# Kernel tuning notes

Measured on AMD Instinct MI355X. Metric: run time of the kernel, lower is better.

The kernel has to match this reference:

```python
import jax, jax.numpy as jnp
import numpy as np
import math

B, S, D, H = 2, 2048, 1024, 16
DH = D // H

def setup_inputs() -> dict:
    key = jax.random.key(0)
    ks = jax.random.split(key, 12)
    s = 1.0 / math.sqrt(D)
    return {
        "q": jax.random.normal(ks[0], (B, S, D), jnp.float32),
        "k": jax.random.normal(ks[1], (B, S, D), jnp.float32),
        "v": jax.random.normal(ks[2], (B, S, D), jnp.float32),
        "mask": jnp.tril(jnp.ones((S, S), dtype=bool)),  # causal mask
        "Wq": jax.random.normal(ks[3], (D, D), jnp.float32) * s,
        "bq": jnp.zeros((D,), jnp.float32),
        "Wk": jax.random.normal(ks[4], (D, D), jnp.float32) * s,
        "bk": jnp.zeros((D,), jnp.float32),
        "Wv": jax.random.normal(ks[5], (D, D), jnp.float32) * s,
        "bv": jnp.zeros((D,), jnp.float32),
        "Wo": jax.random.normal(ks[6], (D, D), jnp.float32) * s,
        "bo": jnp.zeros((D,), jnp.float32),
    }

def _split_heads(x):
    b, s, _ = x.shape
    return x.reshape(b, s, H, DH).transpose(0, 2, 1, 3)  # [B,H,S,DH]

def reference(q, k, v, mask, Wq, bq, Wk, bk, Wv, bv, Wo, bo):
    qh = _split_heads(q @ Wq.T + bq)
    kh = _split_heads(k @ Wk.T + bk)
    vh = _split_heads(v @ Wv.T + bv)
    scale = 1.0 / math.sqrt(DH)
    scores = jnp.einsum('bhqd,bhkd->bhqk', qh, kh) * scale  # [B,H,S,S]
    scores = jnp.where(mask[None, None, :, :], scores, -jnp.inf)
    attn = jax.nn.softmax(scores, axis=-1)
    out = jnp.einsum('bhqk,bhkd->bhqd', attn, vh)  # [B,H,S,DH]
    out = out.transpose(0, 2, 1, 3).reshape(B, S, D)  # combine heads
    return out @ Wo.T + bo
```

## Files before the change

### kernel.cpp

```cpp
#include <hip/hip_runtime.h>

typedef unsigned int u32;
typedef unsigned short u16;
typedef __attribute__((ext_vector_type(8))) short bf16x8;
typedef __attribute__((ext_vector_type(8))) u16 u16x8;
typedef __attribute__((ext_vector_type(4))) u16 u16x4;
typedef __attribute__((ext_vector_type(4))) float f32x4;
typedef __attribute__((ext_vector_type(2))) u32 u32x2;

#define AS1 __attribute__((address_space(1)))
#define AS3 __attribute__((address_space(3)))

__device__ __forceinline__ void gload_lds16(const void* g, void* l) {
  __builtin_amdgcn_global_load_lds((const AS1 u32*)g, (AS3 u32*)l, 16, 0, 0);
}

__device__ __forceinline__ u16 f2bf(float f) {
  union { float f; u32 u; } x; x.f = f;
  u32 u = x.u;
  return (u16)((u + 0x7fffu + ((u >> 16) & 1u)) >> 16);
}

__device__ __forceinline__ u32 cvt_pk_bf16(float lo, float hi) {
  u32 r;
  asm("v_cvt_pk_bf16_f32 %0, %1, %2" : "=v"(r) : "v"(lo), "v"(hi));
  return r;
}

__device__ __forceinline__ float fexp2(float x) {
  float r;
  asm("v_exp_f32 %0, %1" : "=v"(r) : "v"(x));
  return r;
}

__global__ __launch_bounds__(256) void convert_all(
    const float* __restrict__ q, const float* __restrict__ k, const float* __restrict__ v,
    const float* __restrict__ wq, const float* __restrict__ wk,
    const float* __restrict__ wv, const float* __restrict__ wo,
    u16* __restrict__ dst)
{
  int b = blockIdx.x, t = threadIdx.x;
  const float* sp; size_t lb;
  if (b < 6144) {
    sp = (b < 2048) ? q : ((b < 4096) ? k : v);
    lb = (size_t)(b & 2047) * 2048;
  } else {
    int w = (b - 6144) >> 9;
    sp = (w == 0) ? wq : ((w == 1) ? wk : ((w == 2) ? wv : wo));
    lb = (size_t)((b - 6144) & 511) * 2048;
  }
  lb += (size_t)t * 8;
  f32x4 f0 = *(const f32x4*)(sp + lb);
  f32x4 f1 = *(const f32x4*)(sp + lb + 4);
  u16x8 o;
  o[0]=f2bf(f0[0]); o[1]=f2bf(f0[1]); o[2]=f2bf(f0[2]); o[3]=f2bf(f0[3]);
  o[4]=f2bf(f1[0]); o[5]=f2bf(f1[1]); o[6]=f2bf(f1[2]); o[7]=f2bf(f1[3]);
  *(u16x8*)(dst + (size_t)b*2048 + (size_t)t*8) = o;
}

__global__ __launch_bounds__(256, 3) void gemm_qkv(
    const u16* __restrict__ Xall,
    const u16* __restrict__ Wall,
    const float* __restrict__ bq, const float* __restrict__ bk, const float* __restrict__ bv,
    u16* __restrict__ Cqk, u16* __restrict__ VT)
{
  __shared__ __align__(16) u16 lds[24576];
  const int t = threadIdx.x;
  const int wid = t >> 6, l = t & 63;
  const int c = l & 15, g = l >> 4;
  const int u = blockIdx.x;
  const int lid = (u & 7) * 96 + (u >> 3);
  const int which = lid >> 8;
  const int r5 = lid & 255;
  const int m0 = (r5 >> 3) * 128, n0 = (r5 & 7) * 128;
  const u16* A  = Xall + (size_t)which * 4194304;
  const u16* Bw = Wall + (size_t)which * 1048576;
  const int wr = wid >> 1, wc = wid & 1;

  const int srow = wid*16 + (l >> 2);
  const int sswz = ((l & 3) ^ (srow & 3) ^ ((srow >> 2) & 3)) << 3;
  const u16* Asrc0 = A  + (size_t)(m0 + srow)*1024      + sswz;
  const u16* Asrc1 = A  + (size_t)(m0 + 64 + srow)*1024 + sswz;
  const u16* Bsrc0 = Bw + (size_t)(n0 + srow)*1024      + sswz;
  const u16* Bsrc1 = Bw + (size_t)(n0 + 64 + srow)*1024 + sswz;
  const int wbase = wid * 512;

#define QKV_STAGE(j) do { \
    const int bo_ = ((j) % 3) * 8192; const int ko_ = (j) << 5; \
    gload_lds16(Asrc0 + ko_, &lds[bo_ + wbase]); \
    gload_lds16(Asrc1 + ko_, &lds[bo_ + 2048 + wbase]); \
    gload_lds16(Bsrc0 + ko_, &lds[bo_ + 4096 + wbase]); \
    gload_lds16(Bsrc1 + ko_, &lds[bo_ + 6144 + wbase]); \
  } while (0)

  const int fswz = (g ^ (c & 3) ^ ((c >> 2) & 3)) << 3;
  const int abase = (wr*64 + c)*32 + fswz;
  const int bbase = 4096 + (wc*64 + c)*32 + fswz;

  f32x4 acc[4][4] = {};

  QKV_STAGE(0);
  QKV_STAGE(1);
  asm volatile("s_waitcnt vmcnt(4)" ::: "memory");
  __builtin_amdgcn_s_barrier();
  __builtin_amdgcn_sched_barrier(0);

#pragma unroll
  for (int tstep = 0; tstep < 32; ++tstep) {
    if (tstep + 2 < 32) QKV_STAGE(tstep + 2);
    const int bo = (tstep % 3) * 8192;
    bf16x8 af[4], bf[4];
#pragma unroll
    for (int mf = 0; mf < 4; ++mf)
      af[mf] = *(const bf16x8*)&lds[bo + abase + mf*512];
#pragma unroll
    for (int nf = 0; nf < 4; ++nf)
      bf[nf] = *(const bf16x8*)&lds[bo + bbase + nf*512];
    __builtin_amdgcn_s_setprio(1);
#pragma unroll
    for (int mf = 0; mf < 4; ++mf)
#pragma unroll
      for (int nf = 0; nf < 4; ++nf)
        acc[mf][nf] = __builtin_amdgcn_mfma_f32_16x16x32_bf16(af[mf], bf[nf], acc[mf][nf], 0, 0, 0);
    __builtin_amdgcn_s_setprio(0);
    if (tstep + 2 < 32) asm volatile("s_waitcnt vmcnt(4)" ::: "memory");
    else                asm volatile("s_waitcnt vmcnt(0)" ::: "memory");
    __builtin_amdgcn_s_barrier();
    __builtin_amdgcn_sched_barrier(0);
  }
#undef QKV_STAGE

  const float* bias = (which == 0) ? bq : ((which == 1) ? bk : bv);
  if (which < 2) {
#pragma unroll
    for (int mf = 0; mf < 4; ++mf)
#pragma unroll
      for (int nf = 0; nf < 4; ++nf) {
        int row = m0 + wr*64 + mf*16 + g*4;
        int col = n0 + wc*64 + nf*16 + c;
        float bv_ = bias[col];
        int colg = which*1024 + col;
#pragma unroll
        for (int r = 0; r < 4; ++r)
          Cqk[(size_t)(row+r)*2048 + colg] = f2bf(acc[mf][nf][r] + bv_);
      }
  } else {
#pragma unroll
    for (int mf = 0; mf < 4; ++mf)
#pragma unroll
      for (int nf = 0; nf < 4; ++nf) {
        int row = m0 + wr*64 + mf*16 + g*4;
        int col = n0 + wc*64 + nf*16 + c;
        float bv_ = bias[col];
        int bb2 = row >> 11, s = row & 2047;
        int hh = col >> 6, dh = col & 63;
        u16x4 pk;
#pragma unroll
        for (int r = 0; r < 4; ++r) pk[r] = f2bf(acc[mf][nf][r] + bv_);
        *(u16x4*)&VT[((size_t)(((bb2<<4)+hh)<<6) + dh)*2048 + s] = pk;
      }
  }
}

__global__ __launch_bounds__(256, 3) void gemm_out(
    const u16* __restrict__ A, const u16* __restrict__ Bw,
    const float* __restrict__ bias, float* __restrict__ C)
{
  __shared__ __align__(16) u16 lds[24576];
  const int t = threadIdx.x;
  const int wid = t >> 6, l = t & 63;
  const int c = l & 15, g = l >> 4;
  const int u = blockIdx.x;
  const int lid = (u & 7) * 32 + (u >> 3);
  const int m0 = (lid >> 3) * 128, n0 = (lid & 7) * 128;
  const int wr = wid >> 1, wc = wid & 1;

  const int srow = wid*16 + (l >> 2);
  const int sswz = (((l & 3) ^ (srow & 3) ^ ((srow >> 2) & 3)) << 3);
  const u16* Asrc0 = A  + (size_t)(m0 + srow)*1024      + sswz;
  const u16* Asrc1 = A  + (size_t)(m0 + 64 + srow)*1024 + sswz;
  const u16* Bsrc0 = Bw + (size_t)(n0 + srow)*1024      + sswz;
  const u16* Bsrc1 = Bw + (size_t)(n0 + 64 + srow)*1024 + sswz;
  const int wbase = wid * 512;

#define O_STAGE(j) do { \
    const int bo_ = ((j) % 3) * 8192; const int ko_ = (j) << 5; \
    gload_lds16(Asrc0 + ko_, &lds[bo_ + wbase]); \
    gload_lds16(Asrc1 + ko_, &lds[bo_ + 2048 + wbase]); \
    gload_lds16(Bsrc0 + ko_, &lds[bo_ + 4096 + wbase]); \
    gload_lds16(Bsrc1 + ko_, &lds[bo_ + 6144 + wbase]); \
  } while (0)

  const int fswz = (g ^ (c & 3) ^ ((c >> 2) & 3)) << 3;
  const int abase = (wr*64 + c)*32 + fswz;
  const int bbase = 4096 + (wc*64 + c)*32 + fswz;

  f32x4 acc[4][4] = {};

  O_STAGE(0);
  O_STAGE(1);
  asm volatile("s_waitcnt vmcnt(4)" ::: "memory");
  __builtin_amdgcn_s_barrier();
  __builtin_amdgcn_sched_barrier(0);

#pragma unroll
  for (int tstep = 0; tstep < 32; ++tstep) {
    if (tstep + 2 < 32) O_STAGE(tstep + 2);
    const int bo = (tstep % 3) * 8192;
    bf16x8 af[4], bf[4];
#pragma unroll
    for (int mf = 0; mf < 4; ++mf)
      af[mf] = *(const bf16x8*)&lds[bo + abase + mf*512];
#pragma unroll
    for (int nf = 0; nf < 4; ++nf)
      bf[nf] = *(const bf16x8*)&lds[bo + bbase + nf*512];
    __builtin_amdgcn_s_setprio(1);
#pragma unroll
    for (int mf = 0; mf < 4; ++mf)
#pragma unroll
      for (int nf = 0; nf < 4; ++nf)
        acc[mf][nf] = __builtin_amdgcn_mfma_f32_16x16x32_bf16(af[mf], bf[nf], acc[mf][nf], 0, 0, 0);
    __builtin_amdgcn_s_setprio(0);
    if (tstep + 2 < 32) asm volatile("s_waitcnt vmcnt(4)" ::: "memory");
    else                asm volatile("s_waitcnt vmcnt(0)" ::: "memory");
    __builtin_amdgcn_s_barrier();
    __builtin_amdgcn_sched_barrier(0);
  }
#undef O_STAGE

#pragma unroll
  for (int mf = 0; mf < 4; ++mf)
#pragma unroll
    for (int nf = 0; nf < 4; ++nf) {
      int row = m0 + wr*64 + mf*16 + g*4;
      int col = n0 + wc*64 + nf*16 + c;
      float bv_ = bias[col];
#pragma unroll
      for (int r = 0; r < 4; ++r)
        C[(size_t)(row+r)*1024 + col] = acc[mf][nf][r] + bv_;
    }
}

__device__ __forceinline__ void stage_kv(u16* lds, const u16* Kt, const u16* Vt,
                                         int buf, int wid) {
#pragma unroll
  for (int ii = 0; ii < 2; ++ii)
    gload_lds16(Kt + (size_t)ii*32*2048, &lds[4096 + buf*4096 + ii*2048 + wid*512]);
#pragma unroll
  for (int ii = 0; ii < 2; ++ii)
    gload_lds16(Vt + (size_t)ii*32*2048, &lds[12288 + buf*4096 + ii*2048 + wid*512]);
}

__device__ __forceinline__ void attn_phase(
    u16* lds, const u16* Qg, const u16* Ka, const u16* Va,
    int q0, int kt0, int nkv, bool maskLast,
    int wid, int g, int c, int arow, int achk, int pbase, int cs,
    float& MI, float& LI, f32x4 (&o)[4])
{
  const float SC = 0.18033688f;
#pragma unroll
  for (int i = 0; i < 2; ++i) {
    int row = i*32 + arow;
    gload_lds16(Qg + (size_t)(q0+row)*2048 + ((achk ^ (row&7)) << 3),
                &lds[i*2048 + wid*512]);
  }
  const u16* Kt = Ka + (size_t)kt0 * (64*2048);
  const u16* Vt = Va + kt0 * 64;
  stage_kv(lds, Kt, Vt, 0, wid);
  asm volatile("s_waitcnt vmcnt(0)" ::: "memory");
  __builtin_amdgcn_s_barrier();
  __builtin_amdgcn_sched_barrier(0);

  bf16x8 qf[2];
#pragma unroll
  for (int kh = 0; kh < 2; ++kh) {
    int row = wid*16 + c;
    int ch = (kh*4 + g) ^ (row & 7);
    qf[kh] = *(const bf16x8*)&lds[row*64 + ch*8];
  }

  float mi = -INFINITY, li = 0.f;
#pragma unroll
  for (int df = 0; df < 4; ++df) o[df] = f32x4{0.f, 0.f, 0.f, 0.f};

  for (int i = 0; i < nkv; ++i) {
    if (i + 1 < nkv) {
      Kt += 64*2048; Vt += 64;
      stage_kv(lds, Kt, Vt, (i+1)&1, wid);
    }
    const u16* Kb = &lds[4096  + (i&1)*4096];
    const u16* Vb = &lds[12288 + (i&1)*4096];

    f32x4 sT[4] = {};
    __builtin_amdgcn_s_setprio(1);
#pragma unroll
    for (int kh = 0; kh < 2; ++kh) {
      bf16x8 kf[4];
#pragma unroll
      for (int nf = 0; nf < 4; ++nf) {
        int row = nf*16 + c;
        int ch = (kh*4 + g) ^ (c & 7);
        kf[nf] = *(const bf16x8*)&Kb[row*64 + ch*8];
      }
#pragma unroll
      for (int nf = 0; nf < 4; ++nf)
        sT[nf] = __builtin_amdgcn_mfma_f32_16x16x32_bf16(kf[nf], qf[kh], sT[nf], 0,0,0);
    }
    __builtin_amdgcn_s_setprio(0);

    if (maskLast && i == nkv - 1) {
#pragma unroll
      for (int nf = 0; nf < 4; ++nf)
#pragma unroll
        for (int r = 0; r < 4; ++r)
          if (nf*16 + g*4 + r > wid*16 + c) sT[nf][r] = -INFINITY;
    }

    float mx = fmaxf(fmaxf(sT[0][0], sT[0][1]), fmaxf(sT[0][2], sT[0][3]));
#pragma unroll
    for (int nf = 1; nf < 4; ++nf)
      mx = fmaxf(mx, fmaxf(fmaxf(sT[nf][0], sT[nf][1]), fmaxf(sT[nf][2], sT[nf][3])));
    if (!__all(mx * SC <= mi + 8.f)) {
      float mxr = fmaxf(mx, __shfl_xor(mx, 16, 64));
      mxr = fmaxf(mxr, __shfl_xor(mxr, 32, 64));
      float mn = fmaxf(mi, mxr * SC);
      float corr = fexp2(mi - mn);
      li *= corr;
#pragma unroll
      for (int df = 0; df < 4; ++df) {
        o[df][0] *= corr; o[df][1] *= corr;
        o[df][2] *= corr; o[df][3] *= corr;
      }
      mi = mn;
    }
    float sum = 0.f;
#pragma unroll
    for (int nf = 0; nf < 4; ++nf)
#pragma unroll
      for (int r = 0; r < 4; ++r) {
        float pv = fexp2(fmaf(sT[nf][r], SC, -mi));
        sT[nf][r] = pv;
        sum += pv;
      }
    li += sum;

#pragma unroll
    for (int nf = 0; nf < 4; ++nf) {
      u32x2 ww;
      ww[0] = cvt_pk_bf16(sT[nf][0], sT[nf][1]);
      ww[1] = cvt_pk_bf16(sT[nf][2], sT[nf][3]);
      int ch = (2*nf + (g >> 1)) ^ cs;
      *(u32x2*)&lds[pbase + c*64 + ch*8 + (g & 1)*4] = ww;
    }
    asm volatile("s_waitcnt lgkmcnt(0)" ::: "memory");
    __builtin_amdgcn_sched_barrier(0);

    __builtin_amdgcn_s_setprio(1);
#pragma unroll
    for (int kh = 0; kh < 2; ++kh) {
      bf16x8 pfr, vf[4];
      {
        int ch = (kh*4 + g) ^ cs;
        pfr = *(const bf16x8*)&lds[pbase + c*64 + ch*8];
      }
#pragma unroll
      for (int df = 0; df < 4; ++df) {
        int d = df*16 + c;
        int ch = (kh*4 + g) ^ (d & 7);
        vf[df] = *(const bf16x8*)&Vb[d*64 + ch*8];
      }
#pragma unroll
      for (int df = 0; df < 4; ++df)
        o[df] = __builtin_amdgcn_mfma_f32_16x16x32_bf16(vf[df], pfr, o[df], 0,0,0);
    }
    __builtin_amdgcn_s_setprio(0);

    asm volatile("s_waitcnt vmcnt(0)" ::: "memory");
    __builtin_amdgcn_s_barrier();
    __builtin_amdgcn_sched_barrier(0);
  }
  MI = mi; LI = li;
}

__device__ __forceinline__ void store_partial(
    float* __restrict__ part, int slot, int s,
    int wid, int g, int c, float mi, float li_tot, const f32x4 (&o)[4])
{
  float* po = part + (size_t)(slot*2 + s) * 4224;
  int q = wid*16 + c;
#pragma unroll
  for (int df = 0; df < 4; ++df)
    *(f32x4*)&po[q*64 + df*16 + g*4] = o[df];
  if (g == 0) { po[4096 + q] = mi; po[4160 + q] = li_tot; }
}

__global__ __launch_bounds__(256, 4) void attn_fwd(
    const u16* __restrict__ QK, const u16* __restrict__ VT,
    u16* __restrict__ AO, float* __restrict__ part)
{
  __shared__ __align__(16) u16 lds[20480];
  const int t = threadIdx.x;
  const int wid = t >> 6, l = t & 63;
  const int g = l >> 4, c = l & 15;
  const int u = blockIdx.x;
  const int lid = (u & 7) * 128 + (u >> 3);
  const int gx = lid & 31, h = (lid >> 5) & 15, b = lid >> 9;
  const int p = gx >> 1, s = gx & 1;
  const u16* Qg  = QK + (size_t)b * 2048 * 2048 + (size_t)h * 64;
  const u16* Kg  = Qg + 1024;
  const u16* VTg = VT + (size_t)(((b << 4) + h) << 6) * 2048;
  const int arow = t >> 3, achk = t & 7;
  const int pbase = wid * 1024;
  const int cs = (c & 7) ^ ((c >> 3) << 2);
  const u16* Ka = Kg  + (size_t)arow*2048 + ((achk ^ (arow & 7)) << 3);
  const u16* Va = VTg + (size_t)arow*2048 + ((achk ^ (arow & 7)) << 3);
  const int slot = ((b*16 + h)*16 + p);

  float mi, li; f32x4 o[4];

  if (s == 0) {
    attn_phase(lds, Qg, Ka, Va, p*64, 0, p+1, true,
               wid, g, c, arow, achk, pbase, cs, mi, li, o);
    {
      float lt = li + __shfl_xor(li, 16, 64);
      lt += __shfl_xor(lt, 32, 64);
      float nr = 1.f / lt;
      int row = p*64 + wid*16 + c;
      size_t rb = ((size_t)b*2048 + row)*1024 + h*64;
#pragma unroll
      for (int df = 0; df < 4; ++df) {
        u16x4 pk;
        pk[0] = f2bf(o[df][0] * nr); pk[1] = f2bf(o[df][1] * nr);
        pk[2] = f2bf(o[df][2] * nr); pk[3] = f2bf(o[df][3] * nr);
        *(u16x4*)&AO[rb + df*16 + g*4] = pk;
      }
    }
    attn_phase(lds, Qg, Ka, Va, (31-p)*64, 0, 16-p, false,
               wid, g, c, arow, achk, pbase, cs, mi, li, o);
    float lt = li + __shfl_xor(li, 16, 64);
    lt += __shfl_xor(lt, 32, 64);
    store_partial(part, slot, 0, wid, g, c, mi, lt, o);
  } else {
    attn_phase(lds, Qg, Ka, Va, (31-p)*64, 16-p, 16, true,
               wid, g, c, arow, achk, pbase, cs, mi, li, o);
    float lt = li + __shfl_xor(li, 16, 64);
    lt += __shfl_xor(lt, 32, 64);
    store_partial(part, slot, 1, wid, g, c, mi, lt, o);
  }
}

__global__ __launch_bounds__(256) void attn_merge(
    const float* __restrict__ part, u16* __restrict__ AO)
{
  int slot = blockIdx.x;
  int p = slot & 15;
  int h = (slot >> 4) & 15;
  int b = slot >> 8;
  const float* p0 = part + (size_t)slot * 8448;
  const float* p1 = p0 + 4224;
  int t = threadIdx.x;
  int r = t >> 2, c0 = (t & 3) * 16;
  float m0 = p0[4096 + r], m1 = p1[4096 + r];
  float l0 = p0[4160 + r], l1 = p1[4160 + r];
  float m = fmaxf(m0, m1);
  float e0 = exp2f(m0 - m), e1 = exp2f(m1 - m);
  float rl = 1.f / (l0*e0 + l1*e1);
  e0 *= rl; e1 *= rl;
  const f32x4* a0 = (const f32x4*)(p0 + r*64 + c0);
  const f32x4* a1 = (const f32x4*)(p1 + r*64 + c0);
  u16x8 w0, w1;
#pragma unroll
  for (int q4 = 0; q4 < 4; ++q4) {
    f32x4 x = a0[q4], y = a1[q4];
#pragma unroll
    for (int j = 0; j < 4; ++j) {
      u16 bf = f2bf(x[j]*e0 + y[j]*e1);
      if (q4 < 2) w0[q4*4+j] = bf; else w1[(q4-2)*4+j] = bf;
    }
  }
  int qrow = (31 - p)*64 + r;
  size_t ab = ((size_t)b*2048 + qrow)*1024 + h*64 + c0;
  *(u16x8*)&AO[ab]     = w0;
  *(u16x8*)&AO[ab + 8] = w1;
}

extern "C" void kernel_launch(void* const* d_in, const int* in_sizes, int n_in,
                              void* d_out, int out_size, void* d_ws, size_t ws_size,
                              hipStream_t stream)
{
  const float* q  = (const float*)d_in[0];
  const float* k  = (const float*)d_in[1];
  const float* v  = (const float*)d_in[2];
  const float* Wq = (const float*)d_in[4];
  const float* bq = (const float*)d_in[5];
  const float* Wk = (const float*)d_in[6];
  const float* bk = (const float*)d_in[7];
  const float* Wv = (const float*)d_in[8];
  const float* bv = (const float*)d_in[9];
  const float* Wo = (const float*)d_in[10];
  const float* bo = (const float*)d_in[11];
  float* out = (float*)d_out;

  u16* ws   = (u16*)d_ws;
  u16* qb   = ws;
  u16* Wqb  = ws + 12582912;
  u16* Wob  = ws + 15728640;
  u16* QKp  = ws + 16777216;
  u16* VTp  = ws + 25165824;
  u16* AO   = ws + 29360128;

  convert_all<<<8192, 256, 0, stream>>>(q, k, v, Wq, Wk, Wv, Wo, qb);

  gemm_qkv<<<768, 256, 0, stream>>>(qb, Wqb, bq, bk, bv, QKp, VTp);

  attn_fwd<<<1024, 256, 0, stream>>>(QKp, VTp, AO, (float*)d_ws);

  attn_merge<<<512, 256, 0, stream>>>((const float*)d_ws, AO);

  gemm_out<<<256, 256, 0, stream>>>(AO, Wob, bo, out);
}
```

Measured before the change: 106.4 us.

## Load V and Q fragments directly from global, shrink LDS and raise occupancy

Q fragments are now read straight from global memory into registers, and V fragments are loaded per iteration from global instead of being staged through double-buffered LDS. Only K stays staged in LDS. This cuts LDS use from 40KB to 24KB per block, and launch bounds rise from 4 to 6 blocks per CU for more occupancy. The trade-off is that uncoalesced, latency-exposed global loads for V sit in the inner loop, and the larger occupancy target puts more pressure on registers.

```diff
diff --git a/kernel.cpp b/kernel.cpp
--- a/kernel.cpp
+++ b/kernel.cpp
@@ -241,72 +241,68 @@
     }
 }
 
-__device__ __forceinline__ void stage_kv(u16* lds, const u16* Kt, const u16* Vt,
-                                         int buf, int wid) {
+__device__ __forceinline__ void stage_k(u16* lds, const u16* Kt, int buf, int wid) {
 #pragma unroll
   for (int ii = 0; ii < 2; ++ii)
     gload_lds16(Kt + (size_t)ii*32*2048, &lds[4096 + buf*4096 + ii*2048 + wid*512]);
-#pragma unroll
-  for (int ii = 0; ii < 2; ++ii)
-    gload_lds16(Vt + (size_t)ii*32*2048, &lds[12288 + buf*4096 + ii*2048 + wid*512]);
 }
 
 __device__ __forceinline__ void attn_phase(
-    u16* lds, const u16* Qg, const u16* Ka, const u16* Va,
+    u16* lds, const u16* Qg, const u16* Ka, const u16* Vl,
     int q0, int kt0, int nkv, bool maskLast,
-    int wid, int g, int c, int arow, int achk, int pbase, int cs,
+    int wid, int g, int c, int pbase, int cs,
     float& MI, float& LI, f32x4 (&o)[4])
 {
   const float SC = 0.18033688f;
-#pragma unroll
-  for (int i = 0; i < 2; ++i) {
-    int row = i*32 + arow;
-    gload_lds16(Qg + (size_t)(q0+row)*2048 + ((achk ^ (row&7)) << 3),
-                &lds[i*2048 + wid*512]);
-  }
+  const u16* Qrow = Qg + (size_t)(q0 + wid*16 + c) * 2048;
+  bf16x8 qf0 = *(const bf16x8*)(Qrow + g*8);
+  bf16x8 qf1 = *(const bf16x8*)(Qrow + 32 + g*8);
+
   const u16* Kt = Ka + (size_t)kt0 * (64*2048);
-  const u16* Vt = Va + kt0 * 64;
-  stage_kv(lds, Kt, Vt, 0, wid);
+  const u16* Vp = Vl + kt0 * 64;
+  stage_k(lds, Kt, 0, wid);
   asm volatile("s_waitcnt vmcnt(0)" ::: "memory");
   __builtin_amdgcn_s_barrier();
   __builtin_amdgcn_sched_barrier(0);
 
-  bf16x8 qf[2];
-#pragma unroll
-  for (int kh = 0; kh < 2; ++kh) {
-    int row = wid*16 + c;
-    int ch = (kh*4 + g) ^ (row & 7);
-    qf[kh] = *(const bf16x8*)&lds[row*64 + ch*8];
-  }
-
   float mi = -INFINITY, li = 0.f;
 #pragma unroll
   for (int df = 0; df < 4; ++df) o[df] = f32x4{0.f, 0.f, 0.f, 0.f};
 
   for (int i = 0; i < nkv; ++i) {
     if (i + 1 < nkv) {
-      Kt += 64*2048; Vt += 64;
-      stage_kv(lds, Kt, Vt, (i+1)&1, wid);
-    }
-    const u16* Kb = &lds[4096  + (i&1)*4096];
-    const u16* Vb = &lds[12288 + (i&1)*4096];
+      Kt += 64*2048;
+      stage_k(lds, Kt, (i+1)&1, wid);
+    }
+    const u16* Kb = &lds[4096 + (i&1)*4096];
 
     f32x4 sT[4] = {};
     __builtin_amdgcn_s_setprio(1);
-#pragma unroll
-    for (int kh = 0; kh < 2; ++kh) {
+    {
       bf16x8 kf[4];
 #pragma unroll
       for (int nf = 0; nf < 4; ++nf) {
-        int row = nf*16 + c;
-        int ch = (kh*4 + g) ^ (c & 7);
-        kf[nf] = *(const bf16x8*)&Kb[row*64 + ch*8];
+        int ch = g ^ (c & 7);
+        kf[nf] = *(const bf16x8*)&Kb[(nf*16 + c)*64 + ch*8];
       }
 #pragma unroll
       for (int nf = 0; nf < 4; ++nf)
-        sT[nf] = __builtin_amdgcn_mfma_f32_16x16x32_bf16(kf[nf], qf[kh], sT[nf], 0,0,0);
+        sT[nf] = __builtin_amdgcn_mfma_f32_16x16x32_bf16(kf[nf], qf0, sT[nf], 0,0,0);
+#pragma unroll
+      for (int nf = 0; nf < 4; ++nf) {
+        int ch = (4 + g) ^ (c & 7);
+        kf[nf] = *(const bf16x8*)&Kb[(nf*16 + c)*64 + ch*8];
+      }
+#pragma unroll
+      for (int nf = 0; nf < 4; ++nf)
+        sT[nf] = __builtin_amdgcn_mfma_f32_16x16x32_bf16(kf[nf], qf1, sT[nf], 0,0,0);
     }
     __builtin_amdgcn_s_setprio(0);
+
+    bf16x8 vfa[4];
+#pragma unroll
+    for (int df = 0; df < 4; ++df)
+      vfa[df] = *(const bf16x8*)(Vp + (size_t)df*32768);
 
     if (maskLast && i == nkv - 1) {
 #pragma unroll
@@ -352,32 +348,33 @@
       int ch = (2*nf + (g >> 1)) ^ cs;
       *(u32x2*)&lds[pbase + c*64 + ch*8 + (g & 1)*4] = ww;
     }
+
+    bf16x8 vfb[4];
+#pragma unroll
+    for (int df = 0; df < 4; ++df)
+      vfb[df] = *(const bf16x8*)(Vp + (size_t)df*32768 + 32);
+
     asm volatile("s_waitcnt lgkmcnt(0)" ::: "memory");
     __builtin_amdgcn_sched_barrier(0);
 
     __builtin_amdgcn_s_setprio(1);
-#pragma unroll
-    for (int kh = 0; kh < 2; ++kh) {
-      bf16x8 pfr, vf[4];
-      {
-        int ch = (kh*4 + g) ^ cs;
-        pfr = *(const bf16x8*)&lds[pbase + c*64 + ch*8];
-      }
-#pragma unroll
-      for (int df = 0; df < 4; ++df) {
-        int d = df*16 + c;
-        int ch = (kh*4 + g) ^ (d & 7);
-        vf[df] = *(const bf16x8*)&Vb[d*64 + ch*8];
-      }
+    {
+      bf16x8 pfr;
+      { int ch = g ^ cs; pfr = *(const bf16x8*)&lds[pbase + c*64 + ch*8]; }
 #pragma unroll
       for (int df = 0; df < 4; ++df)
-        o[df] = __builtin_amdgcn_mfma_f32_16x16x32_bf16(vf[df], pfr, o[df], 0,0,0);
+        o[df] = __builtin_amdgcn_mfma_f32_16x16x32_bf16(vfa[df], pfr, o[df], 0,0,0);
+      { int ch = (4 + g) ^ cs; pfr = *(const bf16x8*)&lds[pbase + c*64 + ch*8]; }
+#pragma unroll
+      for (int df = 0; df < 4; ++df)
+        o[df] = __builtin_amdgcn_mfma_f32_16x16x32_bf16(vfb[df], pfr, o[df], 0,0,0);
     }
     __builtin_amdgcn_s_setprio(0);
 
     asm volatile("s_waitcnt vmcnt(0)" ::: "memory");
     __builtin_amdgcn_s_barrier();
     __builtin_amdgcn_sched_barrier(0);
+    Vp += 64;
   }
   MI = mi; LI = li;
 }
@@ -394,11 +391,11 @@
   if (g == 0) { po[4096 + q] = mi; po[4160 + q] = li_tot; }
 }
 
-__global__ __launch_bounds__(256, 4) void attn_fwd(
+__global__ __launch_bounds__(256, 6) void attn_fwd(
     const u16* __restrict__ QK, const u16* __restrict__ VT,
     u16* __restrict__ AO, float* __restrict__ part)
 {
-  __shared__ __align__(16) u16 lds[20480];
+  __shared__ __align__(16) u16 lds[12288];
   const int t = threadIdx.x;
   const int wid = t >> 6, l = t & 63;
   const int g = l >> 4, c = l & 15;
@@ -413,14 +410,14 @@
   const int pbase = wid * 1024;
   const int cs = (c & 7) ^ ((c >> 3) << 2);
   const u16* Ka = Kg  + (size_t)arow*2048 + ((achk ^ (arow & 7)) << 3);
-  const u16* Va = VTg + (size_t)arow*2048 + ((achk ^ (arow & 7)) << 3);
+  const u16* Vl = VTg + (size_t)c*2048 + g*8;
   const int slot = ((b*16 + h)*16 + p);
 
   float mi, li; f32x4 o[4];
 
   if (s == 0) {
-    attn_phase(lds, Qg, Ka, Va, p*64, 0, p+1, true,
-               wid, g, c, arow, achk, pbase, cs, mi, li, o);
+    attn_phase(lds, Qg, Ka, Vl, p*64, 0, p+1, true,
+               wid, g, c, pbase, cs, mi, li, o);
     {
       float lt = li + __shfl_xor(li, 16, 64);
       lt += __shfl_xor(lt, 32, 64);
@@ -435,14 +432,14 @@
         *(u16x4*)&AO[rb + df*16 + g*4] = pk;
       }
     }
-    attn_phase(lds, Qg, Ka, Va, (31-p)*64, 0, 16-p, false,
-               wid, g, c, arow, achk, pbase, cs, mi, li, o);
+    attn_phase(lds, Qg, Ka, Vl, (31-p)*64, 0, 16-p, false,
+               wid, g, c, pbase, cs, mi, li, o);
     float lt = li + __shfl_xor(li, 16, 64);
     lt += __shfl_xor(lt, 32, 64);
     store_partial(part, slot, 0, wid, g, c, mi, lt, o);
   } else {
-    attn_phase(lds, Qg, Ka, Va, (31-p)*64, 16-p, 16, true,
-               wid, g, c, arow, achk, pbase, cs, mi, li, o);
+    attn_phase(lds, Qg, Ka, Vl, (31-p)*64, 16-p, 16, true,
+               wid, g, c, pbase, cs, mi, li, o);
     float lt = li + __shfl_xor(li, 16, 64);
     lt += __shfl_xor(lt, 32, 64);
     store_partial(part, slot, 1, wid, g, c, mi, lt, o);
```

After: 155.4 us. +46.0%, slower.
